# Optimization experiments

Measured on AMD Instinct MI355X. Metric: run time of the kernel, lower is better.

Reference implementation:

```python
import jax, jax.numpy as jnp
import numpy as np

KMAX = 0.1  # module init kwarg

def _get_positive_k(k, n):
    if k <= 0:
        return 0
    elif k < 1:
        return round(k * n)
    elif k > n:
        return int(n)
    else:
        return int(k)

def setup_inputs() -> dict:
    key = jax.random.key(0)
    x = jax.random.normal(key, (64, 256, 64, 64), dtype=jnp.float32)
    return {"x": x}

def reference(x):
    b, c, h, w = x.shape
    n = h * w
    k = _get_positive_k(KMAX, n)  # static python int
    flat = x.reshape(b, c, n)
    topv, _ = jax.lax.top_k(flat, k)  # [b, c, k] — partial selection, no full sort materialized
    return topv.sum(axis=2) / k  # [b, c]
```

## Files before the change

### kernel.cpp

```cpp
#include <hip/hip_runtime.h>


#define N_PER_ROW 4096
#define K_SEL 410
#define NROWS (64 * 256)

__device__ __forceinline__ unsigned f2k(float f) {
    unsigned u = __float_as_uint(f);
    unsigned mask = ((unsigned)((int)u >> 31)) | 0x80000000u;
    return u ^ mask;
}
__device__ __forceinline__ float k2f(unsigned key) {
    unsigned u = (key & 0x80000000u) ? (key ^ 0x80000000u) : ~key;
    return __uint_as_float(u);
}

__global__ __launch_bounds__(256) void topk_mean_kernel(const float* __restrict__ x,
                                                        float* __restrict__ out) {
    __shared__ unsigned hist[4 * 256];
    __shared__ unsigned sel_bin_s;
    __shared__ unsigned sel_krem_s;
    __shared__ float wsum[4];

    const int tid  = threadIdx.x;
    const int wid  = tid >> 6;
    const int lane = tid & 63;
    const int row  = blockIdx.x;

    const float4* rowp = (const float4*)(x + (size_t)row * N_PER_ROW);

    unsigned keys[16];
#pragma unroll
    for (int j = 0; j < 4; ++j) {
        float4 v = rowp[j * 256 + tid];
        keys[4 * j + 0] = f2k(v.x);
        keys[4 * j + 1] = f2k(v.y);
        keys[4 * j + 2] = f2k(v.z);
        keys[4 * j + 3] = f2k(v.w);
    }

    unsigned prefix = 0;
    unsigned krem   = K_SEL;

#pragma unroll
    for (int p = 0; p < 4; ++p) {
        const int shift = 24 - 8 * p;
#pragma unroll
        for (int i = 0; i < 4; ++i) hist[i * 256 + tid] = 0;
        __syncthreads();

        unsigned* myh = &hist[wid * 256];
#pragma unroll
        for (int j = 0; j < 16; ++j) {
            unsigned key = keys[j];
            bool part = (p == 0) || ((key >> ((shift + 8) & 31)) == prefix);
            if (part) atomicAdd(&myh[(key >> shift) & 255u], 1u);
        }
        __syncthreads();

        if (tid < 64) {
            const int b0 = lane * 4;
            unsigned h0 = hist[b0 + 0] + hist[256 + b0 + 0] + hist[512 + b0 + 0] + hist[768 + b0 + 0];
            unsigned h1 = hist[b0 + 1] + hist[256 + b0 + 1] + hist[512 + b0 + 1] + hist[768 + b0 + 1];
            unsigned h2 = hist[b0 + 2] + hist[256 + b0 + 2] + hist[512 + b0 + 2] + hist[768 + b0 + 2];
            unsigned h3 = hist[b0 + 3] + hist[256 + b0 + 3] + hist[512 + b0 + 3] + hist[768 + b0 + 3];
            unsigned s3 = h3;
            unsigned s2 = h2 + s3;
            unsigned s1 = h1 + s2;
            unsigned s0 = h0 + s1;
            unsigned tot = s0;
            unsigned suf = tot;
#pragma unroll
            for (int off = 1; off < 64; off <<= 1) {
                unsigned v = __shfl_down(suf, off, 64);
                if (lane + off < 64) suf += v;
            }
            unsigned above = suf - tot;
            unsigned cge0 = s0 + above, cge1 = s1 + above, cge2 = s2 + above, cge3 = s3 + above;
            if (cge0 >= krem && cge0 - h0 < krem) { sel_bin_s = (unsigned)b0 + 0; sel_krem_s = krem - (cge0 - h0); }
            if (cge1 >= krem && cge1 - h1 < krem) { sel_bin_s = (unsigned)b0 + 1; sel_krem_s = krem - (cge1 - h1); }
            if (cge2 >= krem && cge2 - h2 < krem) { sel_bin_s = (unsigned)b0 + 2; sel_krem_s = krem - (cge2 - h2); }
            if (cge3 >= krem && cge3 - h3 < krem) { sel_bin_s = (unsigned)b0 + 3; sel_krem_s = krem - (cge3 - h3); }
        }
        __syncthreads();
        prefix = (prefix << 8) | sel_bin_s;
        krem   = sel_krem_s;
    }

    const unsigned T = prefix;
    float s = 0.0f;
#pragma unroll
    for (int j = 0; j < 16; ++j) {
        if (keys[j] > T) s += k2f(keys[j]);
    }
#pragma unroll
    for (int off = 32; off >= 1; off >>= 1) s += __shfl_xor(s, off, 64);
    if (lane == 0) wsum[wid] = s;
    __syncthreads();
    if (tid == 0) {
        float total = wsum[0] + wsum[1] + wsum[2] + wsum[3] + (float)krem * k2f(T);
        out[row] = total * (1.0f / (float)K_SEL);
    }
}

extern "C" void kernel_launch(void* const* d_in, const int* in_sizes, int n_in,
                              void* d_out, int out_size, void* d_ws, size_t ws_size,
                              hipStream_t stream) {
    const float* x = (const float*)d_in[0];
    float* out = (float*)d_out;
    topk_mean_kernel<<<NROWS, 256, 0, stream>>>(x, out);
}
```

Before: 376.7 us.

## Use 11/11/10-bit radix passes with a block-wide scan instead of four 8-bit passes

Replaces the four 8-bit radix-select passes with three passes over 11, 11 and 10 key bits, using one shared 2048-bin histogram instead of per-wave 256-bin copies. The bin scan now runs across all 256 threads, with a wave-level suffix scan plus a cross-wave total exchange. This removes one full pass of histogram clearing, atomics and barriers. In exchange, all waves contend on a single histogram, so atomic collisions rise, and each pass adds an extra barrier for the cross-wave totals.

```diff
diff --git a/kernel.cpp b/kernel.cpp
--- a/kernel.cpp
+++ b/kernel.cpp
@@ -4,6 +4,7 @@
 #define N_PER_ROW 4096
 #define K_SEL 410
 #define NROWS (64 * 256)
+#define NBINS 2048
 
 __device__ __forceinline__ unsigned f2k(float f) {
     unsigned u = __float_as_uint(f);
@@ -17,7 +18,8 @@
 
 __global__ __launch_bounds__(256) void topk_mean_kernel(const float* __restrict__ x,
                                                         float* __restrict__ out) {
-    __shared__ unsigned hist[4 * 256];
+    __shared__ __align__(16) unsigned cnt[NBINS];
+    __shared__ unsigned wtot[4];
     __shared__ unsigned sel_bin_s;
     __shared__ unsigned sel_krem_s;
     __shared__ float wsum[4];
@@ -43,47 +45,57 @@
     unsigned krem   = K_SEL;
 
 #pragma unroll
-    for (int p = 0; p < 4; ++p) {
-        const int shift = 24 - 8 * p;
-#pragma unroll
-        for (int i = 0; i < 4; ++i) hist[i * 256 + tid] = 0;
+    for (int p = 0; p < 3; ++p) {
+        *(uint4*)&cnt[8 * tid]     = make_uint4(0, 0, 0, 0);
+        *(uint4*)&cnt[8 * tid + 4] = make_uint4(0, 0, 0, 0);
         __syncthreads();
 
-        unsigned* myh = &hist[wid * 256];
 #pragma unroll
         for (int j = 0; j < 16; ++j) {
             unsigned key = keys[j];
-            bool part = (p == 0) || ((key >> ((shift + 8) & 31)) == prefix);
-            if (part) atomicAdd(&myh[(key >> shift) & 255u], 1u);
+            unsigned b;
+            bool part;
+            if (p == 0)      { part = true;                       b = key >> 21; }
+            else if (p == 1) { part = ((key >> 21) == prefix);    b = (key >> 10) & 0x7FFu; }
+            else             { part = ((key >> 10) == prefix);    b = key & 0x3FFu; }
+            if (part) atomicAdd(&cnt[b], 1u);
         }
         __syncthreads();
 
-        if (tid < 64) {
-            const int b0 = lane * 4;
-            unsigned h0 = hist[b0 + 0] + hist[256 + b0 + 0] + hist[512 + b0 + 0] + hist[768 + b0 + 0];
-            unsigned h1 = hist[b0 + 1] + hist[256 + b0 + 1] + hist[512 + b0 + 1] + hist[768 + b0 + 1];
-            unsigned h2 = hist[b0 + 2] + hist[256 + b0 + 2] + hist[512 + b0 + 2] + hist[768 + b0 + 2];
-            unsigned h3 = hist[b0 + 3] + hist[256 + b0 + 3] + hist[512 + b0 + 3] + hist[768 + b0 + 3];
-            unsigned s3 = h3;
-            unsigned s2 = h2 + s3;
-            unsigned s1 = h1 + s2;
-            unsigned s0 = h0 + s1;
-            unsigned tot = s0;
-            unsigned suf = tot;
+        uint4 c0 = *(const uint4*)&cnt[8 * tid];
+        uint4 c1 = *(const uint4*)&cnt[8 * tid + 4];
+        unsigned h0 = c0.x, h1 = c0.y, h2 = c0.z, h3 = c0.w;
+        unsigned h4 = c1.x, h5 = c1.y, h6 = c1.z, h7 = c1.w;
+        unsigned s7 = h7;
+        unsigned s6 = h6 + s7, s5 = h5 + s6, s4 = h4 + s5;
+        unsigned s3 = h3 + s4, s2 = h2 + s3, s1 = h1 + s2, s0 = h0 + s1;
+        unsigned tot = s0;
+
+        unsigned suf = tot;
 #pragma unroll
-            for (int off = 1; off < 64; off <<= 1) {
-                unsigned v = __shfl_down(suf, off, 64);
-                if (lane + off < 64) suf += v;
-            }
-            unsigned above = suf - tot;
-            unsigned cge0 = s0 + above, cge1 = s1 + above, cge2 = s2 + above, cge3 = s3 + above;
-            if (cge0 >= krem && cge0 - h0 < krem) { sel_bin_s = (unsigned)b0 + 0; sel_krem_s = krem - (cge0 - h0); }
-            if (cge1 >= krem && cge1 - h1 < krem) { sel_bin_s = (unsigned)b0 + 1; sel_krem_s = krem - (cge1 - h1); }
-            if (cge2 >= krem && cge2 - h2 < krem) { sel_bin_s = (unsigned)b0 + 2; sel_krem_s = krem - (cge2 - h2); }
-            if (cge3 >= krem && cge3 - h3 < krem) { sel_bin_s = (unsigned)b0 + 3; sel_krem_s = krem - (cge3 - h3); }
+        for (int off = 1; off < 64; off <<= 1) {
+            unsigned v = __shfl_down(suf, off, 64);
+            if (lane + off < 64) suf += v;
         }
+        if (lane == 0) wtot[wid] = suf;
         __syncthreads();
-        prefix = (prefix << 8) | sel_bin_s;
+
+        unsigned above = suf - tot;
+        for (int w = wid + 1; w < 4; ++w) above += wtot[w];
+
+        const unsigned b0 = 8u * (unsigned)tid;
+        unsigned cg;
+        cg = s0 + above; if (cg >= krem && cg - h0 < krem) { sel_bin_s = b0 + 0; sel_krem_s = krem - (cg - h0); }
+        cg = s1 + above; if (cg >= krem && cg - h1 < krem) { sel_bin_s = b0 + 1; sel_krem_s = krem - (cg - h1); }
+        cg = s2 + above; if (cg >= krem && cg - h2 < krem) { sel_bin_s = b0 + 2; sel_krem_s = krem - (cg - h2); }
+        cg = s3 + above; if (cg >= krem && cg - h3 < krem) { sel_bin_s = b0 + 3; sel_krem_s = krem - (cg - h3); }
+        cg = s4 + above; if (cg >= krem && cg - h4 < krem) { sel_bin_s = b0 + 4; sel_krem_s = krem - (cg - h4); }
+        cg = s5 + above; if (cg >= krem && cg - h5 < krem) { sel_bin_s = b0 + 5; sel_krem_s = krem - (cg - h5); }
+        cg = s6 + above; if (cg >= krem && cg - h6 < krem) { sel_bin_s = b0 + 6; sel_krem_s = krem - (cg - h6); }
+        cg = s7 + above; if (cg >= krem && cg - h7 < krem) { sel_bin_s = b0 + 7; sel_krem_s = krem - (cg - h7); }
+        __syncthreads();
+
+        prefix = (prefix << (p == 2 ? 10 : 11)) | sel_bin_s;
         krem   = sel_krem_s;
     }
 
```

After: 354.6 us. 1.06x faster.

## Assign one wavefront per row with two 11-bit radix passes and no block barriers

Applied to the files above, without the earlier changes.

Each 256-thread block now handles four rows, one per 64-lane wavefront. Every lane holds 64 keys, and each wavefront uses its own padded 2048-bin LDS histogram. Radix selection drops from four 8-bit passes to two 11-bit passes. Block-wide __syncthreads and the shared-memory broadcast are replaced by wavefront-local ballot/shuffle selection. The threshold is then resolved only to 22 bits, so tied elements in the final bin are credited at a bin-midpoint value instead of exactly. This adds a small approximation error and extra register pressure from the 64 keys per lane.

```diff
diff --git a/kernel.cpp b/kernel.cpp
--- a/kernel.cpp
+++ b/kernel.cpp
@@ -1,38 +1,36 @@
 #include <hip/hip_runtime.h>
 
 
-#define N_PER_ROW 4096
 #define K_SEL 410
 #define NROWS (64 * 256)
+#define ROWLEN 4096
+#define PADB (2048 + 64)
 
 __device__ __forceinline__ unsigned f2k(float f) {
     unsigned u = __float_as_uint(f);
-    unsigned mask = ((unsigned)((int)u >> 31)) | 0x80000000u;
-    return u ^ mask;
+    return u ^ (((unsigned)((int)u >> 31)) | 0x80000000u);
 }
 __device__ __forceinline__ float k2f(unsigned key) {
-    unsigned u = (key & 0x80000000u) ? (key ^ 0x80000000u) : ~key;
+    unsigned u = key ^ (0x80000000u | ~(unsigned)((int)key >> 31));
     return __uint_as_float(u);
 }
 
-__global__ __launch_bounds__(256) void topk_mean_kernel(const float* __restrict__ x,
-                                                        float* __restrict__ out) {
-    __shared__ unsigned hist[4 * 256];
-    __shared__ unsigned sel_bin_s;
-    __shared__ unsigned sel_krem_s;
-    __shared__ float wsum[4];
+__global__ __launch_bounds__(256, 4) void topk_mean_kernel(
+        const float* __restrict__ x, float* __restrict__ out) {
+    __shared__ unsigned hist[4 * PADB];
 
     const int tid  = threadIdx.x;
     const int wid  = tid >> 6;
     const int lane = tid & 63;
-    const int row  = blockIdx.x;
+    const int row  = blockIdx.x * 4 + wid;
 
-    const float4* rowp = (const float4*)(x + (size_t)row * N_PER_ROW);
+    unsigned* h = &hist[wid * PADB];
+    const float4* rowp = (const float4*)(x + (size_t)row * ROWLEN);
 
-    unsigned keys[16];
+    unsigned keys[64];
 #pragma unroll
-    for (int j = 0; j < 4; ++j) {
-        float4 v = rowp[j * 256 + tid];
+    for (int j = 0; j < 16; ++j) {
+        float4 v = rowp[j * 64 + lane];
         keys[4 * j + 0] = f2k(v.x);
         keys[4 * j + 1] = f2k(v.y);
         keys[4 * j + 2] = f2k(v.z);
@@ -43,64 +41,69 @@
     unsigned krem   = K_SEL;
 
 #pragma unroll
-    for (int p = 0; p < 4; ++p) {
-        const int shift = 24 - 8 * p;
+    for (int p = 0; p < 2; ++p) {
 #pragma unroll
-        for (int i = 0; i < 4; ++i) hist[i * 256 + tid] = 0;
-        __syncthreads();
+        for (int j = 0; j < 33; ++j) h[lane + 64 * j] = 0;
+        __threadfence_block();
 
-        unsigned* myh = &hist[wid * 256];
 #pragma unroll
-        for (int j = 0; j < 16; ++j) {
+        for (int j = 0; j < 64; ++j) {
             unsigned key = keys[j];
-            bool part = (p == 0) || ((key >> ((shift + 8) & 31)) == prefix);
-            if (part) atomicAdd(&myh[(key >> shift) & 255u], 1u);
+            unsigned b = (p == 0) ? (key >> 21) : ((key >> 10) & 0x7FFu);
+            bool part = (p == 0) || ((key >> 21) == prefix);
+            if (part) atomicAdd(&h[b + (b >> 5)], 1u);
         }
-        __syncthreads();
+        __threadfence_block();
 
-        if (tid < 64) {
-            const int b0 = lane * 4;
-            unsigned h0 = hist[b0 + 0] + hist[256 + b0 + 0] + hist[512 + b0 + 0] + hist[768 + b0 + 0];
-            unsigned h1 = hist[b0 + 1] + hist[256 + b0 + 1] + hist[512 + b0 + 1] + hist[768 + b0 + 1];
-            unsigned h2 = hist[b0 + 2] + hist[256 + b0 + 2] + hist[512 + b0 + 2] + hist[768 + b0 + 2];
-            unsigned h3 = hist[b0 + 3] + hist[256 + b0 + 3] + hist[512 + b0 + 3] + hist[768 + b0 + 3];
-            unsigned s3 = h3;
-            unsigned s2 = h2 + s3;
-            unsigned s1 = h1 + s2;
-            unsigned s0 = h0 + s1;
-            unsigned tot = s0;
-            unsigned suf = tot;
+        const int base = 33 * lane;
+        unsigned tot = 0;
 #pragma unroll
-            for (int off = 1; off < 64; off <<= 1) {
-                unsigned v = __shfl_down(suf, off, 64);
-                if (lane + off < 64) suf += v;
+        for (int j = 0; j < 32; ++j) tot += h[base + j];
+
+        unsigned suf = tot;
+#pragma unroll
+        for (int off = 1; off < 64; off <<= 1) {
+            unsigned v = __shfl_down(suf, off, 64);
+            if (lane + off < 64) suf += v;
+        }
+        unsigned above = suf - tot;
+
+        bool lane_has = (above < krem) && (suf >= krem);
+
+        unsigned ge = above;
+        unsigned selbin = 0, selkrem = 0;
+        bool found = false;
+#pragma unroll
+        for (int j = 31; j >= 0; --j) {
+            unsigned hj  = h[base + j];
+            unsigned nge = ge + hj;
+            if (!found && nge >= krem) {
+                selbin  = 32u * (unsigned)lane + (unsigned)j;
+                selkrem = krem - ge;
+                found   = true;
             }
-            unsigned above = suf - tot;
-            unsigned cge0 = s0 + above, cge1 = s1 + above, cge2 = s2 + above, cge3 = s3 + above;
-            if (cge0 >= krem && cge0 - h0 < krem) { sel_bin_s = (unsigned)b0 + 0; sel_krem_s = krem - (cge0 - h0); }
-            if (cge1 >= krem && cge1 - h1 < krem) { sel_bin_s = (unsigned)b0 + 1; sel_krem_s = krem - (cge1 - h1); }
-            if (cge2 >= krem && cge2 - h2 < krem) { sel_bin_s = (unsigned)b0 + 2; sel_krem_s = krem - (cge2 - h2); }
-            if (cge3 >= krem && cge3 - h3 < krem) { sel_bin_s = (unsigned)b0 + 3; sel_krem_s = krem - (cge3 - h3); }
+            ge = nge;
         }
-        __syncthreads();
-        prefix = (prefix << 8) | sel_bin_s;
-        krem   = sel_krem_s;
+
+        unsigned long long mvote = __ballot(lane_has && found);
+        int src = (int)__builtin_ctzll(mvote);
+        unsigned sb = (unsigned)__shfl((int)selbin, src, 64);
+        krem        = (unsigned)__shfl((int)selkrem, src, 64);
+        prefix = (p == 0) ? sb : ((prefix << 11) | sb);
     }
 
-    const unsigned T = prefix;
+    const unsigned T22 = prefix;
     float s = 0.0f;
 #pragma unroll
-    for (int j = 0; j < 16; ++j) {
-        if (keys[j] > T) s += k2f(keys[j]);
+    for (int j = 0; j < 64; ++j) {
+        unsigned key = keys[j];
+        if ((key >> 10) > T22) s += k2f(key);
     }
+    if (lane == 0) s += (float)krem * k2f((T22 << 10) | 512u);
+
 #pragma unroll
     for (int off = 32; off >= 1; off >>= 1) s += __shfl_xor(s, off, 64);
-    if (lane == 0) wsum[wid] = s;
-    __syncthreads();
-    if (tid == 0) {
-        float total = wsum[0] + wsum[1] + wsum[2] + wsum[3] + (float)krem * k2f(T);
-        out[row] = total * (1.0f / (float)K_SEL);
-    }
+    if (lane == 0) out[row] = s * (1.0f / (float)K_SEL);
 }
 
 extern "C" void kernel_launch(void* const* d_in, const int* in_sizes, int n_in,
@@ -108,5 +111,5 @@
                               hipStream_t stream) {
     const float* x = (const float*)d_in[0];
     float* out = (float*)d_out;
-    topk_mean_kernel<<<NROWS, 256, 0, stream>>>(x, out);
+    topk_mean_kernel<<<NROWS / 4, 256, 0, stream>>>(x, out);
 }
```

New measurement: 364.5 us. 3.2% less time.
